# Optimization experiments

Measured on AMD Instinct MI355X. Metric: run time of the kernel, lower is better.

Reference implementation:

```python
import jax, jax.numpy as jnp
import numpy as np

SCALE = 0.125  # (dim // heads) ** -0.5 = (256 // 4) ** -0.5


def setup_inputs() -> dict:
    key = jax.random.key(0)
    k1, k2, k3, k4, k5 = jax.random.split(key, 5)
    dim, red = 256, 4
    c = dim // red  # 64
    B, H, W = 4, 64, 64
    x = jax.random.normal(k1, (B, dim, H, W), dtype=jnp.float32)
    qkv_w = jax.random.normal(k2, (3 * c, dim), dtype=jnp.float32) * 0.02
    qkv_b = jax.random.normal(k3, (3 * c,), dtype=jnp.float32) * 0.02
    proj_w = jax.random.normal(k4, (dim, c), dtype=jnp.float32) * 0.02
    proj_b = jax.random.normal(k5, (dim,), dtype=jnp.float32) * 0.02
    return {"x": x, "qkv_w": qkv_w, "qkv_b": qkv_b, "proj_w": proj_w, "proj_b": proj_b}


def reference(x, qkv_w, qkv_b, proj_w, proj_b):
    B, C, H, W = x.shape
    # 1x1 conv == channel matmul
    qkv = jnp.einsum('bchw,oc->bohw', x, qkv_w) + qkv_b[None, :, None, None]
    c = qkv.shape[1] // 3
    qkv = qkv.reshape(B, 3 * c, H * W)
    q, k, v = qkv[:, :c], qkv[:, c:2 * c], qkv[:, 2 * c:]  # [B, c, HW]
    # attn[b, n, m] = sum_c q[b,c,n] * k[b,c,m] * scale
    attn = jnp.einsum('bcn,bcm->bnm', q, k) * SCALE
    attn = jax.nn.softmax(attn, axis=-1)  # [B, HW, HW]
    # out[b, c, n] = sum_m v[b,c,m] * attn[b,n,m]   (v @ attn^T)
    out = jnp.einsum('bcm,bnm->bcn', v, attn).reshape(B, c, H, W)
    # proj 1x1 conv back to dim
    return jnp.einsum('bchw,oc->bohw', out, proj_w) + proj_b[None, :, None, None]
```

## Files before the change

kernel.cpp:

```cpp
#include <hip/hip_runtime.h>
#include <hip/hip_bf16.h>


#define N_TOK 4096
#define CDIM  64
#define DIM   256
#define NBAT  4

typedef __attribute__((ext_vector_type(8)))  short          short8;
typedef __attribute__((ext_vector_type(8)))  unsigned short ushort8_t;
typedef __attribute__((ext_vector_type(4)))  unsigned short ushort4_t;
typedef __attribute__((ext_vector_type(4)))  unsigned int   uint4_t;
typedef __attribute__((ext_vector_type(4)))  float          float4_t;
typedef __attribute__((ext_vector_type(16))) float          float16_t;

#if __has_builtin(__builtin_amdgcn_exp2f)
#define QSC  0.18033688011112042f
#define PEXP(x) __builtin_amdgcn_exp2f(x)
#else
#define QSC  0.125f
#define PEXP(x) __expf(x)
#endif

__device__ __forceinline__ unsigned short f2bf(float f) {
  unsigned int u = __builtin_bit_cast(unsigned int, f);
  u += 0x7fffu + ((u >> 16) & 1u);
  return (unsigned short)(u >> 16);
}

__device__ __forceinline__ unsigned int pkcv(float a, float b) {
  __hip_bfloat162 h = __float22bfloat162_rn(make_float2(a, b));
  unsigned int r; __builtin_memcpy(&r, &h, 4); return r;
}

__device__ __forceinline__ short8 ld8(const unsigned short* p) {
  return __builtin_bit_cast(short8, *(const ushort8_t*)p);
}

__device__ __forceinline__ short8 pack8f(float4_t a, float4_t b) {
  uint4_t u;
  u[0] = pkcv(a[0], a[1]); u[1] = pkcv(a[2], a[3]);
  u[2] = pkcv(b[0], b[1]); u[3] = pkcv(b[2], b[3]);
  return __builtin_bit_cast(short8, u);
}

__device__ __forceinline__ float16_t z16() {
  float16_t r;
#pragma unroll
  for (int i = 0; i < 16; ++i) r[i] = 0.0f;
  return r;
}

typedef __attribute__((address_space(1))) const void* gvp;
typedef __attribute__((address_space(3))) void*       lvp;
__device__ __forceinline__ void dma16(const unsigned short* g, unsigned short* l) {
  __builtin_amdgcn_global_load_lds((gvp)g, (lvp)l, 16, 0, 0);
}

#define MFMA(a, b, c) __builtin_amdgcn_mfma_f32_32x32x16_bf16((a), (b), (c), 0, 0, 0)

#define QOFF  0
#define KOFF  1048576
#define VOFF  2097152
#define WQOFF 3145728
#define BSOFF 3194880

__global__ void k_prep(const float* __restrict__ qw, const float* __restrict__ qb,
                       unsigned short* __restrict__ wqs, float* __restrict__ bs)
{
  const int g = blockIdx.x * 256 + threadIdx.x;
  {
    const int lane = g & 63, grp = g >> 6;
    const int w6 = grp >> 4, kk = grp & 15;
    const int o = w6 * 32 + (lane & 31);
    const int c = kk * 16 + (lane >> 5) * 8;
    const float sc = (o < 64) ? QSC : 1.0f;
    const float* src = qw + o * 256 + c;
    ushort8_t u;
#pragma unroll
    for (int j = 0; j < 8; ++j) u[j] = f2bf(src[j] * sc);
    *(ushort8_t*)(wqs + g * 8) = u;
  }
  if (g < 48) {
    float4_t f = *(const float4_t*)(qb + g * 4);
    float4_t o;
#pragma unroll
    for (int j = 0; j < 4; ++j) o[j] = f[j] * ((g * 4 + j) < 64 ? QSC : 1.0f);
    *(float4_t*)(bs + g * 4) = o;
  }
}

#define RS 132

__global__ __launch_bounds__(768, 3) void k_qkv(
    const float* __restrict__ x, const unsigned short* __restrict__ wqs,
    const float* __restrict__ bs, unsigned short* __restrict__ Qf,
    unsigned short* __restrict__ Kf, unsigned short* __restrict__ Vf)
{
  __shared__ unsigned int Xl[64 * RS];
  const int id = blockIdx.x;
  const int b  = (id >> 1) & 3;
  const int nt = (id & 1) | ((id >> 3) << 1);
  const int t  = threadIdx.x;
  const int n0g = nt * 64;

  if (t < 512) {
    const int n0  = (t & 15) * 4;
    const int cpb = t >> 4;
#pragma unroll
    for (int p = 0; p < 4; ++p) {
      const int cp = cpb + 32 * p, c = cp * 2;
      const float* xb = x + (((size_t)(b * DIM + c)) << 12) + n0g + n0;
      float4_t a = *(const float4_t*)xb;
      float4_t d = *(const float4_t*)(xb + 4096);
#pragma unroll
      for (int j = 0; j < 4; ++j)
        Xl[(n0 + j) * RS + cp] = pkcv(a[j], d[j]);
    }
  }

  const int w = t >> 6, lane = t & 63, l31 = lane & 31, lh = lane >> 5;
  const int ot = w >> 1, sub = w & 1;
  const int ch = nt * 2 + sub;

  const unsigned short* wrow = wqs + ((ot * 16) << 9) + lane * 8;
  short8 wf[16];
#pragma unroll
  for (int kk = 0; kk < 16; ++kk) wf[kk] = ld8(wrow + (kk << 9));

  __syncthreads();

  const unsigned int* xr = &Xl[(sub * 32 + l31) * RS + lh * 4];

  float16_t a0 = z16();
  if (ot < 4) {
#pragma unroll
    for (int kk = 0; kk < 16; ++kk) {
      short8 xf = __builtin_bit_cast(short8, *(const uint4_t*)(xr + kk * 8));
      a0 = MFMA(wf[kk], xf, a0);
    }
  } else {
#pragma unroll
    for (int kk = 0; kk < 16; ++kk) {
      short8 xf = __builtin_bit_cast(short8, *(const uint4_t*)(xr + kk * 8));
      a0 = MFMA(xf, wf[kk], a0);
    }
  }

  if (ot < 4) {
    unsigned short* dst = (ot < 2) ? Qf : Kf;
    const int w2 = ot & 1;
#pragma unroll
    for (int p = 0; p < 4; ++p) {
      const int o = ot * 32 + p * 8 + lh * 4;
      float4_t bv = *(const float4_t*)(bs + o);
      ushort4_t pk4;
#pragma unroll
      for (int q = 0; q < 4; ++q) pk4[q] = f2bf(a0[p * 4 + q] + bv[q]);
      const int kkt = w2 * 2 + (p >> 1);
      *(ushort4_t*)(dst + ((((b * 128 + ch) * 4 + kkt) << 9)
                           + (l31 + 32 * (p & 1)) * 8 + lh * 4)) = pk4;
    }
  } else {
    const int ct = ot - 4;
    const float bvs = bs[128 + ct * 32 + l31];
#pragma unroll
    for (int ks = 0; ks < 2; ++ks) {
      ushort8_t pk8;
#pragma unroll
      for (int j = 0; j < 8; ++j) pk8[j] = f2bf(a0[ks * 8 + j] + bvs);
      *(ushort8_t*)(Vf + ((((b * 128 + ch) * 4 + ct * 2 + ks) << 9)
                          + lane * 8)) = pk8;
    }
  }
}

#define OS   68
#define OLS  72
#define NACC (64 * OS + 64)

__global__ __launch_bounds__(512, 1) void k_attn(
    const unsigned short* __restrict__ Qf, const unsigned short* __restrict__ Kf,
    const unsigned short* __restrict__ Vf, const float* __restrict__ pw,
    const float* __restrict__ pb, float* __restrict__ out)
{
  __shared__ __align__(16) unsigned short Kl[2][32768];
  __shared__ float Oacc[NACC];
  __shared__ __align__(16) unsigned short Ol[64 * OLS];

  const int id = blockIdx.x;
  const int b  = (id >> 1) & 3;
  const int nt = (id & 1) | ((id >> 3) << 1);
  const int t  = threadIdx.x;
  const int wv = t >> 6, lane = t & 63, l31 = lane & 31, lh = lane >> 5;
  const int mq = wv >> 1, nsub = wv & 1;

  for (int i = t; i < NACC; i += 512) Oacc[i] = 0.0f;

  const int wq2 = wv * 2;
  const unsigned short* sg = Kf + (((size_t)(b * 128 + wq2)) << 11) + lane * 8;

  short8 qf[4];
#pragma unroll
  for (int kk = 0; kk < 4; ++kk)
    qf[kk] = ld8(Qf + (((b * 128 + nt * 2 + nsub) * 4 + kk) << 9) + lane * 8);

  const unsigned short* vbase = Vf + (((size_t)(b * 128)) << 11) + lane * 8;

#pragma unroll
  for (int c2 = 0; c2 < 2; ++c2)
#pragma unroll
    for (int kk = 0; kk < 4; ++kk)
      dma16(sg + (c2 << 11) + (kk << 9),
            &Kl[0][((wq2 + c2) << 11) + (kk << 9)]);

  float16_t oc0 = z16(), oc1 = z16();
  float den = 0.0f;

  __syncthreads();

  for (int t8 = 0; t8 < 8; ++t8) {
    const int cur = t8 & 1;

    if (t8 < 7) {
      const unsigned short* g = sg + (((size_t)(t8 + 1)) << 15);
#pragma unroll
      for (int c2 = 0; c2 < 2; ++c2)
#pragma unroll
        for (int kk = 0; kk < 4; ++kk)
          dma16(g + (c2 << 11) + (kk << 9),
                &Kl[cur ^ 1][((wq2 + c2) << 11) + (kk << 9)]);
    }

#pragma unroll
    for (int cc = 0; cc < 4; ++cc) {
      const int ch = mq * 4 + cc;
      const unsigned short* kl = &Kl[cur][ch << 11];

      short8 kf0 = ld8(kl + lane * 8);
      short8 kf1 = ld8(kl + 512 + lane * 8);
      short8 kf2 = ld8(kl + 1024 + lane * 8);
      short8 kf3 = ld8(kl + 1536 + lane * 8);

      float16_t s = z16();
      s = MFMA(kf0, qf[0], s);
      s = MFMA(kf1, qf[1], s);
      s = MFMA(kf2, qf[2], s);
      s = MFMA(kf3, qf[3], s);

      float p[16];
#pragma unroll
      for (int e = 0; e < 16; ++e) p[e] = PEXP(s[e]);
      {
        float d0 = (p[0] + p[1]) + (p[2] + p[3]);
        float d1 = (p[4] + p[5]) + (p[6] + p[7]);
        float d2 = (p[8] + p[9]) + (p[10] + p[11]);
        float d3 = (p[12] + p[13]) + (p[14] + p[15]);
        den += (d0 + d1) + (d2 + d3);
      }

      uint4_t w0, w1;
#pragma unroll
      for (int j = 0; j < 4; ++j) {
        w0[j] = pkcv(p[2 * j], p[2 * j + 1]);
        w1[j] = pkcv(p[8 + 2 * j], p[9 + 2 * j]);
      }
      short8 pf0 = __builtin_bit_cast(short8, w0);
      short8 pf1 = __builtin_bit_cast(short8, w1);

      const unsigned short* vl = vbase + (((size_t)(t8 * 16 + ch)) << 11);
      short8 vf0 = ld8(vl);
      short8 vf1 = ld8(vl + 512);
      short8 vf2 = ld8(vl + 1024);
      short8 vf3 = ld8(vl + 1536);

      oc0 = MFMA(pf0, vf0, oc0);
      oc0 = MFMA(pf1, vf1, oc0);
      oc1 = MFMA(pf0, vf2, oc1);
      oc1 = MFMA(pf1, vf3, oc1);
    }

    __syncthreads();
  }

  den += __shfl_xor(den, 32);

#pragma unroll
  for (int ct = 0; ct < 2; ++ct) {
    const float16_t& oa = ct ? oc1 : oc0;
    const int cc = ct * 32 + l31;
#pragma unroll
    for (int e = 0; e < 16; ++e) {
      const int nr = nsub * 32 + (e & 3) + 8 * (e >> 2) + 4 * lh;
      atomicAdd(&Oacc[nr * OS + cc], oa[e]);
    }
  }
  if (lane < 32) atomicAdd(&Oacc[64 * OS + nsub * 32 + l31], den);
  __syncthreads();

  {
    const int nloc = t >> 3, c8 = (t & 7) * 8;
    float4_t s0 = *(float4_t*)&Oacc[nloc * OS + c8];
    float4_t s1 = *(float4_t*)&Oacc[nloc * OS + c8 + 4];
    const float r = 1.0f / Oacc[64 * OS + nloc];
    uint4_t o4;
    o4[0] = pkcv(s0[0] * r, s0[1] * r);
    o4[1] = pkcv(s0[2] * r, s0[3] * r);
    o4[2] = pkcv(s1[0] * r, s1[1] * r);
    o4[3] = pkcv(s1[2] * r, s1[3] * r);
    *(uint4_t*)&Ol[nloc * OLS + c8] = o4;
  }
  __syncthreads();

  float16_t f0 = z16(), f1 = z16();
  const float* pwrow = pw + (wv * 32 + l31) * 64 + lh * 8;
#pragma unroll
  for (int kk = 0; kk < 4; ++kk) {
    float4_t wa = *(const float4_t*)(pwrow + kk * 16);
    float4_t wb = *(const float4_t*)(pwrow + kk * 16 + 4);
    short8 af = pack8f(wa, wb);
    short8 b0 = ld8(&Ol[l31 * OLS + kk * 16 + lh * 8]);
    short8 b1 = ld8(&Ol[(32 + l31) * OLS + kk * 16 + lh * 8]);
    f0 = MFMA(af, b0, f0);
    f1 = MFMA(af, b1, f1);
  }
  const int n0 = nt * 64;
#pragma unroll
  for (int e = 0; e < 16; ++e) {
    const int o = wv * 32 + (e & 3) + 8 * (e >> 2) + 4 * lh;
    const float bv = pb[o];
    out[((b * 256 + o) << 12) + n0 + l31]      = f0[e] + bv;
    out[((b * 256 + o) << 12) + n0 + 32 + l31] = f1[e] + bv;
  }
}

extern "C" void kernel_launch(void* const* d_in, const int* in_sizes, int n_in,
                              void* d_out, int out_size, void* d_ws, size_t ws_size,
                              hipStream_t stream) {
  const float* x      = (const float*)d_in[0];
  const float* qkv_w  = (const float*)d_in[1];
  const float* qkv_b  = (const float*)d_in[2];
  const float* proj_w = (const float*)d_in[3];
  const float* proj_b = (const float*)d_in[4];
  float* out = (float*)d_out;

  unsigned short* ws  = (unsigned short*)d_ws;
  unsigned short* qf  = ws + QOFF;
  unsigned short* kf  = ws + KOFF;
  unsigned short* vf  = ws + VOFF;
  unsigned short* wqs = ws + WQOFF;
  float*          bs  = (float*)(ws + BSOFF);

  k_prep<<<24, 256, 0, stream>>>(qkv_w, qkv_b, wqs, bs);
  k_qkv<<<256, 768, 0, stream>>>(x, wqs, bs, qf, kf, vf);
  k_attn<<<256, 512, 0, stream>>>(qf, kf, vf, proj_w, proj_b, out);
}
```

Baseline: 131.0 us.

## Split attention over key chunks with a separate combine-and-project kernel

Replaces the single fused attention kernel with a split-K style scheme. Each block handles 256 queries against a quarter of the keys, double-buffering K and V tiles into LDS via direct global-to-LDS loads. It writes unnormalized fp32 partial outputs and softmax denominators to workspace. A second kernel sums the four partials, normalizes, and applies the projection with MFMA. The aim is to shorten the per-block serial loop over keys, at the cost of extra global traffic for the fp32 partials and one more launch. It still uses exp without max subtraction. The new path runs only when the workspace is large enough, otherwise it falls back to the old kernel.

```diff
diff --git a/kernel.cpp b/kernel.cpp
--- a/kernel.cpp
+++ b/kernel.cpp
@@ -64,6 +64,9 @@
 #define VOFF  2097152
 #define WQOFF 3145728
 #define BSOFF 3194880
+#define OPOFF 3276800
+#define DNOFF (OPOFF + 8388608)
+#define WS_NEED_U16 (DNOFF + 131072)
 
 __global__ void k_prep(const float* __restrict__ qw, const float* __restrict__ qb,
                        unsigned short* __restrict__ wqs, float* __restrict__ bs)
@@ -136,14 +139,14 @@
   if (ot < 4) {
 #pragma unroll
     for (int kk = 0; kk < 16; ++kk) {
-      short8 xf = __builtin_bit_cast(short8, *(const uint4_t*)(xr + kk * 8));
-      a0 = MFMA(wf[kk], xf, a0);
+      short8 xv = __builtin_bit_cast(short8, *(const uint4_t*)(xr + kk * 8));
+      a0 = MFMA(wf[kk], xv, a0);
     }
   } else {
 #pragma unroll
     for (int kk = 0; kk < 16; ++kk) {
-      short8 xf = __builtin_bit_cast(short8, *(const uint4_t*)(xr + kk * 8));
-      a0 = MFMA(xf, wf[kk], a0);
+      short8 xv = __builtin_bit_cast(short8, *(const uint4_t*)(xr + kk * 8));
+      a0 = MFMA(xv, wf[kk], a0);
     }
   }
 
@@ -175,8 +178,180 @@
   }
 }
 
+__global__ __launch_bounds__(512, 1) void k_attn_p(
+    const unsigned short* __restrict__ Qf, const unsigned short* __restrict__ Kf,
+    const unsigned short* __restrict__ Vf, float* __restrict__ Opart,
+    float* __restrict__ denp)
+{
+  __shared__ __align__(16) unsigned short KV[2][2][16384];
+
+  const int id = blockIdx.x;
+  const int b  = (id >> 1) & 3;
+  const int v  = (id & 1) | ((id >> 3) << 1);
+  const int qt = v >> 2;
+  const int ks = v & 3;
+  const int t  = threadIdx.x;
+  const int wv = t >> 6, lane = t & 63, l31 = lane & 31, lh = lane >> 5;
+
+  const int cq = qt * 8 + wv;
+  short8 qf[4];
+#pragma unroll
+  for (int kk = 0; kk < 4; ++kk)
+    qf[kk] = ld8(Qf + (((b * 128 + cq) * 4 + kk) << 9) + lane * 8);
+
+  const unsigned short* sgK = Kf + (((size_t)(b * 128 + ks * 32 + wv)) << 11) + lane * 8;
+  const unsigned short* sgV = Vf + (((size_t)(b * 128 + ks * 32 + wv)) << 11) + lane * 8;
+
+#pragma unroll
+  for (int kk = 0; kk < 4; ++kk)
+    dma16(sgK + (kk << 9), &KV[0][0][(wv << 11) + (kk << 9)]);
+#pragma unroll
+  for (int kk = 0; kk < 4; ++kk)
+    dma16(sgV + (kk << 9), &KV[0][1][(wv << 11) + (kk << 9)]);
+
+  float16_t oc0 = z16(), oc1 = z16();
+  float den = 0.0f;
+
+  __syncthreads();
+
+  for (int t4 = 0; t4 < 4; ++t4) {
+    const int cur = t4 & 1;
+
+    if (t4 < 3) {
+      const size_t go = ((size_t)(t4 + 1)) << 14;
+#pragma unroll
+      for (int kk = 0; kk < 4; ++kk)
+        dma16(sgK + go + (kk << 9), &KV[cur ^ 1][0][(wv << 11) + (kk << 9)]);
+#pragma unroll
+      for (int kk = 0; kk < 4; ++kk)
+        dma16(sgV + go + (kk << 9), &KV[cur ^ 1][1][(wv << 11) + (kk << 9)]);
+    }
+
+#pragma unroll
+    for (int cc = 0; cc < 8; ++cc) {
+      const unsigned short* kl = &KV[cur][0][cc << 11];
+      const unsigned short* vl = &KV[cur][1][cc << 11];
+
+      short8 kf0 = ld8(kl + lane * 8);
+      short8 kf1 = ld8(kl + 512 + lane * 8);
+      short8 kf2 = ld8(kl + 1024 + lane * 8);
+      short8 kf3 = ld8(kl + 1536 + lane * 8);
+
+      float16_t s = z16();
+      s = MFMA(kf0, qf[0], s);
+      s = MFMA(kf1, qf[1], s);
+      s = MFMA(kf2, qf[2], s);
+      s = MFMA(kf3, qf[3], s);
+
+      float p[16];
+#pragma unroll
+      for (int e = 0; e < 16; ++e) p[e] = PEXP(s[e]);
+      {
+        float d0 = (p[0] + p[1]) + (p[2] + p[3]);
+        float d1 = (p[4] + p[5]) + (p[6] + p[7]);
+        float d2 = (p[8] + p[9]) + (p[10] + p[11]);
+        float d3 = (p[12] + p[13]) + (p[14] + p[15]);
+        den += (d0 + d1) + (d2 + d3);
+      }
+
+      uint4_t w0, w1;
+#pragma unroll
+      for (int j = 0; j < 4; ++j) {
+        w0[j] = pkcv(p[2 * j], p[2 * j + 1]);
+        w1[j] = pkcv(p[8 + 2 * j], p[9 + 2 * j]);
+      }
+      short8 pf0 = __builtin_bit_cast(short8, w0);
+      short8 pf1 = __builtin_bit_cast(short8, w1);
+
+      short8 vf0 = ld8(vl + lane * 8);
+      short8 vf1 = ld8(vl + 512 + lane * 8);
+      short8 vf2 = ld8(vl + 1024 + lane * 8);
+      short8 vf3 = ld8(vl + 1536 + lane * 8);
+
+      oc0 = MFMA(pf0, vf0, oc0);
+      oc0 = MFMA(pf1, vf1, oc0);
+      oc1 = MFMA(pf0, vf2, oc1);
+      oc1 = MFMA(pf1, vf3, oc1);
+    }
+
+    __syncthreads();
+  }
+
+  den += __shfl_xor(den, 32);
+
+  float* op = Opart + (((size_t)(ks * 4 + b) * 4096) + qt * 256 + wv * 32) * 64;
+#pragma unroll
+  for (int e = 0; e < 16; ++e) {
+    const int r = (e & 3) + 8 * (e >> 2) + 4 * lh;
+    op[r * 64 + l31]      = oc0[e];
+    op[r * 64 + 32 + l31] = oc1[e];
+  }
+  if (lane < 32)
+    denp[((size_t)(ks * 4 + b) * 4096) + qt * 256 + wv * 32 + l31] = den;
+}
+
+#define OLS  72
+
+__global__ __launch_bounds__(512, 2) void k_comb(
+    const float* __restrict__ Opart, const float* __restrict__ denp,
+    const float* __restrict__ pw, const float* __restrict__ pb,
+    float* __restrict__ out)
+{
+  __shared__ __align__(16) unsigned short Ol[64 * OLS];
+
+  const int id = blockIdx.x;
+  const int b  = (id >> 1) & 3;
+  const int nt = (id & 1) | ((id >> 3) << 1);
+  const int t  = threadIdx.x;
+  const int wv = t >> 6, lane = t & 63, l31 = lane & 31, lh = lane >> 5;
+
+  {
+    const int nloc = t >> 3, c8 = (t & 7) * 8;
+    const size_t R = (size_t)nt * 64 + nloc;
+    float4_t s0 = {0.f, 0.f, 0.f, 0.f}, s1 = {0.f, 0.f, 0.f, 0.f};
+    float d = 0.0f;
+#pragma unroll
+    for (int ks = 0; ks < 4; ++ks) {
+      const float* op = Opart + (((size_t)(ks * 4 + b) * 4096) + R) * 64 + c8;
+      float4_t a0 = *(const float4_t*)op;
+      float4_t a1 = *(const float4_t*)(op + 4);
+#pragma unroll
+      for (int j = 0; j < 4; ++j) { s0[j] += a0[j]; s1[j] += a1[j]; }
+      d += denp[((size_t)(ks * 4 + b) * 4096) + R];
+    }
+    const float r = 1.0f / d;
+    uint4_t o4;
+    o4[0] = pkcv(s0[0] * r, s0[1] * r);
+    o4[1] = pkcv(s0[2] * r, s0[3] * r);
+    o4[2] = pkcv(s1[0] * r, s1[1] * r);
+    o4[3] = pkcv(s1[2] * r, s1[3] * r);
+    *(uint4_t*)&Ol[nloc * OLS + c8] = o4;
+  }
+  __syncthreads();
+
+  float16_t f0 = z16(), f1 = z16();
+  const float* pwrow = pw + (wv * 32 + l31) * 64 + lh * 8;
+#pragma unroll
+  for (int kk = 0; kk < 4; ++kk) {
+    float4_t wa = *(const float4_t*)(pwrow + kk * 16);
+    float4_t wb = *(const float4_t*)(pwrow + kk * 16 + 4);
+    short8 af = pack8f(wa, wb);
+    short8 b0 = ld8(&Ol[l31 * OLS + kk * 16 + lh * 8]);
+    short8 b1 = ld8(&Ol[(32 + l31) * OLS + kk * 16 + lh * 8]);
+    f0 = MFMA(af, b0, f0);
+    f1 = MFMA(af, b1, f1);
+  }
+  const int n0 = nt * 64;
+#pragma unroll
+  for (int e = 0; e < 16; ++e) {
+    const int o = wv * 32 + (e & 3) + 8 * (e >> 2) + 4 * lh;
+    const float bv = pb[o];
+    out[((b * 256 + o) << 12) + n0 + l31]      = f0[e] + bv;
+    out[((b * 256 + o) << 12) + n0 + 32 + l31] = f1[e] + bv;
+  }
+}
+
 #define OS   68
-#define OLS  72
 #define NACC (64 * OS + 64)
 
 __global__ __launch_bounds__(512, 1) void k_attn(
@@ -350,8 +525,16 @@
   unsigned short* vf  = ws + VOFF;
   unsigned short* wqs = ws + WQOFF;
   float*          bs  = (float*)(ws + BSOFF);
+  float*          op  = (float*)(ws + OPOFF);
+  float*          dn  = (float*)(ws + DNOFF);
 
   k_prep<<<24, 256, 0, stream>>>(qkv_w, qkv_b, wqs, bs);
   k_qkv<<<256, 768, 0, stream>>>(x, wqs, bs, qf, kf, vf);
-  k_attn<<<256, 512, 0, stream>>>(qf, kf, vf, proj_w, proj_b, out);
-}
+
+  if (ws_size >= (size_t)WS_NEED_U16 * 2) {
+    k_attn_p<<<256, 512, 0, stream>>>(qf, kf, vf, op, dn);
+    k_comb<<<256, 512, 0, stream>>>(op, dn, proj_w, proj_b, out);
+  } else {
+    k_attn<<<256, 512, 0, stream>>>(qf, kf, vf, proj_w, proj_b, out);
+  }
+}
```

Result: faster. 110.0 us (-16.0%).
